# Kernel tuning notes

Hardware: AMD Instinct MI355X
Metric: run time of the kernel (lower is better)

Reference implementation:

```python
import jax, jax.numpy as jnp
import numpy as np

N = 33554432
LABEL = 5
PENALIZE_WEIGHT = 3.0
LOWER = LABEL - 0.5
UPPER = LABEL + 0.5


def setup_inputs() -> dict:
    key = jax.random.key(0)
    k1, k2 = jax.random.split(key)
    x = jax.random.normal(k1, (N,), dtype=jnp.float32)
    t = jax.random.randint(k2, (N,), 0, 10, dtype=jnp.int64)
    return {"input": x, "target": t}


def reference(input, target):
    # Fused elementwise mask: weight = penalize_weight where
    # lower < x < upper AND target != label, else 1.0
    x = input
    penal = (x > LOWER) & (x < UPPER) & (target != LABEL)
    w = jnp.where(penal, jnp.float32(PENALIZE_WEIGHT), jnp.float32(1.0))
    diff = x - target.astype(jnp.float32)
    return jnp.mean(w * diff * diff)
```

## Files before the change

kernel.cpp:

```cpp
#include <hip/hip_runtime.h>


#define LABEL_I   5
#define LOWER_F   4.5f
#define UPPER_F   5.5f
#define PENALTY_F 3.0f

__device__ __forceinline__ float term(float x, int t) {
    float d = x - (float)t;
    float w = (x > LOWER_F && x < UPPER_F && t != LABEL_I) ? PENALTY_F : 1.0f;
    return w * d * d;
}

__device__ __forceinline__ float term4(float4 xv, int4 tv) {
    return term(xv.x, tv.x) + term(xv.y, tv.y) + term(xv.z, tv.z) + term(xv.w, tv.w);
}

__global__ __launch_bounds__(256) void penal_mse_kernel(
        const float4* __restrict__ x4,
        const int4*  __restrict__ t4,
        float* __restrict__ out,
        int n4, float inv_n, int n_tail_start, int n_total,
        const float* __restrict__ x_scalar,
        const int*  __restrict__ t_scalar) {
    int tid    = blockIdx.x * blockDim.x + threadIdx.x;
    int stride = gridDim.x * blockDim.x;

    float s0 = 0.0f, s1 = 0.0f, s2 = 0.0f, s3 = 0.0f;

    int i = tid;
    for (; i + 3 * stride < n4; i += 4 * stride) {
        float4 a0 = x4[i];
        float4 a1 = x4[i + stride];
        float4 a2 = x4[i + 2 * stride];
        float4 a3 = x4[i + 3 * stride];
        int4   b0 = t4[i];
        int4   b1 = t4[i + stride];
        int4   b2 = t4[i + 2 * stride];
        int4   b3 = t4[i + 3 * stride];
        s0 += term4(a0, b0);
        s1 += term4(a1, b1);
        s2 += term4(a2, b2);
        s3 += term4(a3, b3);
    }
    for (; i < n4; i += stride)
        s0 += term4(x4[i], t4[i]);

    float sum = (s0 + s1) + (s2 + s3);

    for (int j = n_tail_start + tid; j < n_total; j += stride)
        sum += term(x_scalar[j], t_scalar[j]);

    #pragma unroll
    for (int off = 32; off > 0; off >>= 1)
        sum += __shfl_down(sum, off, 64);

    __shared__ float wsum[4];
    int lane = threadIdx.x & 63;
    int wave = threadIdx.x >> 6;
    if (lane == 0) wsum[wave] = sum;
    __syncthreads();

    if (threadIdx.x == 0) {
        float bsum = (wsum[0] + wsum[1]) + (wsum[2] + wsum[3]);
        atomicAdd(out, bsum * inv_n);
    }
}

extern "C" void kernel_launch(void* const* d_in, const int* in_sizes, int n_in,
                              void* d_out, int out_size, void* d_ws, size_t ws_size,
                              hipStream_t stream) {
    const float* x = (const float*)d_in[0];
    const int*   t = (const int*)d_in[1];
    float* out = (float*)d_out;

    int n  = in_sizes[0];
    int n4 = n >> 2;
    int n_tail_start = n4 << 2;
    float inv_n = 1.0f / (float)n;

    hipMemsetAsync(d_out, 0, sizeof(float), stream);

    const int block = 256;
    int grid = 2048;
    if (grid > (n4 + block - 1) / block) grid = (n4 + block - 1) / block;
    if (grid < 1) grid = 1;

    penal_mse_kernel<<<grid, block, 0, stream>>>(
        (const float4*)x, (const int4*)t, out,
        n4, inv_n, n_tail_start, n, x, t);
}
```

Measured before the change: 287.1 us.

## Use contiguous per-block tiles and a two-stage reduction instead of memset plus atomics

Each block now reads contiguous 1024-element float4 tiles, four 256-strided loads per thread, instead of a grid-strided pattern. A scheduling barrier keeps all eight loads issued before the arithmetic. The memset and the global atomicAdd are replaced by per-block partials in workspace and a second single-block kernel that sums them. This removes the memset launch and atomic contention but adds a second kernel launch.

After: 273.5 us. 1.05x faster.

```diff
diff --git a/kernel.cpp b/kernel.cpp
--- a/kernel.cpp
+++ b/kernel.cpp
@@ -16,39 +16,42 @@
     return term(xv.x, tv.x) + term(xv.y, tv.y) + term(xv.z, tv.z) + term(xv.w, tv.w);
 }
 
-__global__ __launch_bounds__(256) void penal_mse_kernel(
+#define TPB 1024
+
+__global__ __launch_bounds__(256) void penal_mse_stage1(
         const float4* __restrict__ x4,
         const int4*  __restrict__ t4,
-        float* __restrict__ out,
-        int n4, float inv_n, int n_tail_start, int n_total,
+        float* __restrict__ partials,
+        int n4, int tiles, int n_tail_start, int n_total,
         const float* __restrict__ x_scalar,
         const int*  __restrict__ t_scalar) {
-    int tid    = blockIdx.x * blockDim.x + threadIdx.x;
-    int stride = gridDim.x * blockDim.x;
-
     float s0 = 0.0f, s1 = 0.0f, s2 = 0.0f, s3 = 0.0f;
 
-    int i = tid;
-    for (; i + 3 * stride < n4; i += 4 * stride) {
-        float4 a0 = x4[i];
-        float4 a1 = x4[i + stride];
-        float4 a2 = x4[i + 2 * stride];
-        float4 a3 = x4[i + 3 * stride];
-        int4   b0 = t4[i];
-        int4   b1 = t4[i + stride];
-        int4   b2 = t4[i + 2 * stride];
-        int4   b3 = t4[i + 3 * stride];
+    for (int tile = blockIdx.x; tile < tiles; tile += gridDim.x) {
+        int base = tile * TPB + threadIdx.x;
+        float4 a0 = x4[base];
+        float4 a1 = x4[base + 256];
+        float4 a2 = x4[base + 512];
+        float4 a3 = x4[base + 768];
+        int4   b0 = t4[base];
+        int4   b1 = t4[base + 256];
+        int4   b2 = t4[base + 512];
+        int4   b3 = t4[base + 768];
+        __builtin_amdgcn_sched_barrier(0);
         s0 += term4(a0, b0);
         s1 += term4(a1, b1);
         s2 += term4(a2, b2);
         s3 += term4(a3, b3);
     }
-    for (; i < n4; i += stride)
-        s0 += term4(x4[i], t4[i]);
 
     float sum = (s0 + s1) + (s2 + s3);
 
-    for (int j = n_tail_start + tid; j < n_total; j += stride)
+    for (int i = tiles * TPB + blockIdx.x * blockDim.x + threadIdx.x;
+         i < n4; i += gridDim.x * blockDim.x)
+        sum += term4(x4[i], t4[i]);
+
+    for (int j = n_tail_start + blockIdx.x * blockDim.x + threadIdx.x;
+         j < n_total; j += gridDim.x * blockDim.x)
         sum += term(x_scalar[j], t_scalar[j]);
 
     #pragma unroll
@@ -61,10 +64,29 @@
     if (lane == 0) wsum[wave] = sum;
     __syncthreads();
 
-    if (threadIdx.x == 0) {
-        float bsum = (wsum[0] + wsum[1]) + (wsum[2] + wsum[3]);
-        atomicAdd(out, bsum * inv_n);
-    }
+    if (threadIdx.x == 0)
+        partials[blockIdx.x] = (wsum[0] + wsum[1]) + (wsum[2] + wsum[3]);
+}
+
+__global__ __launch_bounds__(256) void penal_mse_stage2(
+        const float* __restrict__ partials, int nparts,
+        float* __restrict__ out, float inv_n) {
+    float sum = 0.0f;
+    for (int i = threadIdx.x; i < nparts; i += 256)
+        sum += partials[i];
+
+    #pragma unroll
+    for (int off = 32; off > 0; off >>= 1)
+        sum += __shfl_down(sum, off, 64);
+
+    __shared__ float wsum[4];
+    int lane = threadIdx.x & 63;
+    int wave = threadIdx.x >> 6;
+    if (lane == 0) wsum[wave] = sum;
+    __syncthreads();
+
+    if (threadIdx.x == 0)
+        out[0] = ((wsum[0] + wsum[1]) + (wsum[2] + wsum[3])) * inv_n;
 }
 
 extern "C" void kernel_launch(void* const* d_in, const int* in_sizes, int n_in,
@@ -73,20 +95,20 @@
     const float* x = (const float*)d_in[0];
     const int*   t = (const int*)d_in[1];
     float* out = (float*)d_out;
+    float* partials = (float*)d_ws;
 
     int n  = in_sizes[0];
     int n4 = n >> 2;
     int n_tail_start = n4 << 2;
+    int tiles = n4 / TPB;
     float inv_n = 1.0f / (float)n;
 
-    hipMemsetAsync(d_out, 0, sizeof(float), stream);
+    const int block = 256;
+    const int grid = 2048;
 
-    const int block = 256;
-    int grid = 2048;
-    if (grid > (n4 + block - 1) / block) grid = (n4 + block - 1) / block;
-    if (grid < 1) grid = 1;
+    penal_mse_stage1<<<grid, block, 0, stream>>>(
+        (const float4*)x, (const int4*)t, partials,
+        n4, tiles, n_tail_start, n, x, t);
 
-    penal_mse_kernel<<<grid, block, 0, stream>>>(
-        (const float4*)x, (const int4*)t, out,
-        n4, inv_n, n_tail_start, n, x, t);
+    penal_mse_stage2<<<1, block, 0, stream>>>(partials, grid, out, inv_n);
 }
```
